# Kernel optimization log

Measured on AMD Instinct MI355X. Metric: run time of the kernel, lower is better.

The kernel has to match this reference:

```python
import jax, jax.numpy as jnp
import numpy as np

F4_E2M1_MAX = 6.0
F8E4M3_MAX = 448.0
E4M3_EPS = 0.015625  # torch.finfo(float8_e4m3fn).tiny = 2**-6
BLOCK = 16
KE2M1 = jnp.array([0.0, 0.5, 1.0, 1.5, 2.0, 3.0, 4.0, 6.0], dtype=jnp.float32)


def round_to_e4m3(x):
    # emulate cast to float8_e4m3fn and back (round-to-nearest-even)
    return x.astype(jnp.float8_e4m3fn).astype(jnp.float32)


def fp4_121_positive(x):
    step1 = jnp.round(2.0 * x) / 2.0   # subnormal-ish region [0,2): step 0.5
    step2 = jnp.round(x)               # [2,4): step 1
    step3 = 2.0 * jnp.round(x / 2.0)   # [4,6]: step 2
    return jnp.where(x < 2.0, step1, jnp.where(x < 4.0, step2, step3))


def cast_to_fp4(x):
    return jnp.sign(x) * fp4_121_positive(jnp.abs(x))


def unpack_fp4_from_uint8(a, m, n):
    # a: int-typed tensor holding byte values in [0,256); two fp4 codes per byte
    high = (a.reshape(-1) >> 4) & 0xF
    low = a.reshape(-1) & 0xF
    combined = jnp.stack((low, high), axis=1).reshape(m, n)  # interleave low,high
    signs = (combined & 8) != 0
    abs_idx = combined & 7
    return KE2M1[abs_idx] * jnp.where(signs, -1.0, 1.0)


def dequant_nvfp4_packed(data_lp, out_scales, per_tensor_scale):
    m, half_n = data_lp.shape
    n = half_n * 2
    data_hp = unpack_fp4_from_uint8(data_lp, m, n)           # [m, n] float32
    scale_fp = out_scales / per_tensor_scale                  # [m, n/16]
    data_hp = data_hp.reshape(m, -1, BLOCK) * scale_fp.reshape(m, -1, 1)
    return data_hp.reshape(m, n)


def qdq_nvfp4(x):
    m, n = x.shape
    tensor_amax = jnp.max(jnp.abs(x))
    pts = jnp.clip(tensor_amax / F8E4M3_MAX, E4M3_EPS, F8E4M3_MAX)  # per-tensor scale
    xb = x.reshape(m, -1, BLOCK)
    block_scale = jnp.max(jnp.abs(xb), axis=-1) / F4_E2M1_MAX       # [m, n/16]
    scaled_bs = round_to_e4m3(jnp.clip(block_scale / pts, E4M3_EPS, F8E4M3_MAX))
    total_scale = pts * scaled_bs                                   # [m, n/16]
    data_scaled = jnp.clip(xb / total_scale[..., None], -F4_E2M1_MAX, F4_E2M1_MAX)
    data_lp = cast_to_fp4(data_scaled)                              # unpacked fp4 values
    # dequant: out_scales / (1/pts) == scaled_bs * pts == total_scale
    return (data_lp * total_scale[..., None]).reshape(m, n)


def setup_inputs() -> dict:
    key = jax.random.key(0)
    k1, k2, k3 = jax.random.split(key, 3)
    M, K, N = 16384, 2048, 2048  # tokens, in_features, out_features
    x = jax.random.normal(k1, (M, K), dtype=jnp.float32)
    weight_packed = jax.random.randint(k2, (N, K // 2), 0, 256, dtype=jnp.int32)
    # fp8-representable positive block scales
    weight_scale = round_to_e4m3(jax.random.uniform(k3, (N, K // 16), dtype=jnp.float32,
                                                    minval=0.05, maxval=1.0))
    weight_global_scale = jnp.ones((1,), dtype=jnp.float32)
    return {"x": x, "weight_packed": weight_packed,
            "weight_scale": weight_scale, "weight_global_scale": weight_global_scale}


def reference(x, weight_packed, weight_scale, weight_global_scale):
    hp_weight = dequant_nvfp4_packed(weight_packed, weight_scale, weight_global_scale)
    x_dq = qdq_nvfp4(x)
    return x_dq @ hp_weight.T
```

## Files before the change

### kernel.cpp

```cpp
#include <hip/hip_runtime.h>

typedef unsigned short u16;
typedef unsigned int u32;
typedef __attribute__((ext_vector_type(8))) short short8;
typedef __attribute__((ext_vector_type(4))) float floatx4;

static constexpr int M = 16384, N = 2048, K = 2048;


__device__ inline u16 f32_to_bf16(float x) {
    u32 u = __float_as_uint(x);
    u += 0x7FFFu + ((u >> 16) & 1u);
    return (u16)(u >> 16);
}

__device__ inline float e4m3_rne(float x) {
    u32 u = __float_as_uint(x);
    u += 0x7FFFFu + ((u >> 20) & 1u);
    u &= 0xFFF00000u;
    return __uint_as_float(u);
}

__device__ inline float fp4_dec(u32 c) {
    u32 e = (c >> 1) & 3u;
    float m = (float)(c & 1u);
    float v = e ? (2.0f + m) * (float)(1u << e) * 0.25f : 0.5f * m;
    return (c & 8u) ? -v : v;
}

__device__ inline float fp4_round_mag(float a) {
    if (a < 2.0f) return rintf(2.0f * a) * 0.5f;
    if (a < 4.0f) return rintf(a);
    return 2.0f * rintf(a * 0.5f);
}

__device__ inline float pts_from_amax(float amax) {
    return fminf(fmaxf(amax / 448.0f, 0.015625f), 448.0f);
}


__global__ void amax_part(const float4* __restrict__ x, float* __restrict__ part, int n4,
                          const int* __restrict__ wp, const float* __restrict__ wsc,
                          const float* __restrict__ wgs, u16* __restrict__ wq) {
    int idx = blockIdx.x * blockDim.x + threadIdx.x;
    int stride = gridDim.x * blockDim.x;
    float m = 0.0f;
    for (int i = idx; i < n4; i += stride) {
        float4 v = x[i];
        m = fmaxf(m, fmaxf(fmaxf(fabsf(v.x), fabsf(v.y)), fmaxf(fabsf(v.z), fabsf(v.w))));
    }

    float ginv = wgs[0];
#pragma unroll
    for (int g = 0; g < 4; g++) {
        int i = idx + g * 524288;
        int n = i >> 10;
        int kb = i & 1023;
        u32 byte = (u32)wp[i] & 0xFFu;
        float scale = wsc[(size_t)n * (K / 16) + (kb >> 3)] / ginv;
        float lo = fp4_dec(byte & 0xFu) * scale;
        float hi = fp4_dec((byte >> 4) & 0xFu) * scale;
        ((u32*)wq)[i] = (u32)f32_to_bf16(lo) | ((u32)f32_to_bf16(hi) << 16);
    }

#pragma unroll
    for (int off = 32; off > 0; off >>= 1)
        m = fmaxf(m, __shfl_down(m, off));
    __shared__ float sm[4];
    if ((threadIdx.x & 63) == 0) sm[threadIdx.x >> 6] = m;
    __syncthreads();
    if (threadIdx.x == 0)
        part[blockIdx.x] = fmaxf(fmaxf(sm[0], sm[1]), fmaxf(sm[2], sm[3]));
}


__global__ void amax_fin(const float* __restrict__ part, u32* __restrict__ out) {
    int t = threadIdx.x;
    float m = fmaxf(part[t], part[t + 1024]);
#pragma unroll
    for (int off = 32; off > 0; off >>= 1)
        m = fmaxf(m, __shfl_down(m, off));
    __shared__ float sm[16];
    if ((t & 63) == 0) sm[t >> 6] = m;
    __syncthreads();
    if (t < 16) {
        m = sm[t];
#pragma unroll
        for (int off = 8; off > 0; off >>= 1)
            m = fmaxf(m, __shfl_down(m, off));
        if (t == 0) *out = __float_as_uint(m);
    }
}


static constexpr int QB = (M * K / 4) / 256;

__global__ void prep(const float4* __restrict__ x, uint2* __restrict__ aq,
                     const u32* __restrict__ amax_bits) {
    int idx = blockIdx.x * blockDim.x + threadIdx.x;
    float4 v = x[idx];

    float bm = fmaxf(fmaxf(fabsf(v.x), fabsf(v.y)), fmaxf(fabsf(v.z), fabsf(v.w)));
    bm = fmaxf(bm, __shfl_xor(bm, 1));
    bm = fmaxf(bm, __shfl_xor(bm, 2));

    float pts = pts_from_amax(__uint_as_float(*amax_bits));
    float bs = bm / 6.0f;
    float sbs = e4m3_rne(fminf(fmaxf(bs / pts, 0.015625f), 448.0f));
    float ts = pts * sbs;

    float vf[4] = {v.x, v.y, v.z, v.w};
    u16 o[4];
#pragma unroll
    for (int i = 0; i < 4; i++) {
        float s = vf[i] / ts;
        s = fminf(fmaxf(s, -6.0f), 6.0f);
        float lp = copysignf(fp4_round_mag(fabsf(s)), s);
        o[i] = f32_to_bf16(lp * sbs);
    }
    aq[idx] = *(const uint2*)o;
}


#define GLDS(g, l)                                                              \
    __builtin_amdgcn_global_load_lds(                                           \
        (const __attribute__((address_space(1))) unsigned int*)(g),             \
        (__attribute__((address_space(3))) unsigned int*)(l), 16, 0, 0)

__global__ __launch_bounds__(512, 2) void gemm_bt(
    const u16* __restrict__ A, const u16* __restrict__ B,
    float* __restrict__ C, const u32* __restrict__ amax_bits, int bm_base)
{
    __shared__ u16 sh[2][2][2][8192];

    const int tid = threadIdx.x;
    const int w = tid >> 6, lane = tid & 63;

    const int id = blockIdx.x;
    const int xcd = id & 7;
    const int local = id >> 3;
    const int bm = bm_base + xcd * 4 + (local >> 3);
    const int bn = local & 7;

    const int wm = w >> 2, wn = w & 3;
    const int r16 = lane & 15, q = lane >> 4;

    floatx4 acc[8][4] = {};

    const int swz = (r16 & 7) << 4;
    const int aoff0 = r16 * 64 + (((q * 16) ^ swz) >> 1);
    const int aoff1 = r16 * 64 + (((64 + q * 16) ^ swz) >> 1);

    const int srow8 = lane >> 3;
    const int scol = ((lane & 7) ^ srow8) * 8;
    const u16* gA[2], * gB[2];
    gA[0] = A + (size_t)(bm * 256 + (w * 2 + 0) * 8 + srow8) * K + scol;
    gA[1] = A + (size_t)(bm * 256 + (w * 2 + 1) * 8 + srow8) * K + scol;
    gB[0] = B + (size_t)(bn * 256 + (w * 2 + 0) * 8 + srow8) * K + scol;
    gB[1] = B + (size_t)(bn * 256 + (w * 2 + 1) * 8 + srow8) * K + scol;

#define STG(buf, mat, half, ktc) do {                                           \
        const u16* _s0 = ((mat) ? gB[0] : gA[0]) + (size_t)(half) * 128 * K + (ktc); \
        const u16* _s1 = ((mat) ? gB[1] : gA[1]) + (size_t)(half) * 128 * K + (ktc); \
        GLDS(_s0, &sh[buf][mat][half][w * 1024]);                               \
        GLDS(_s1, &sh[buf][mat][half][w * 1024 + 512]);                         \
    } while (0)

    short8 aF[4][2], bF[4][2];

#define RD_A(buf, Qa) do {                                                      \
        const u16* _ar = &sh[buf][0][wm][(Qa) * 4096];                          \
        _Pragma("unroll") for (int _i = 0; _i < 4; _i++) {                      \
            aF[_i][0] = *(const short8*)(_ar + _i * 1024 + aoff0);              \
            aF[_i][1] = *(const short8*)(_ar + _i * 1024 + aoff1); }            \
    } while (0)

#define RD_B(buf, Qb) do {                                                      \
        const u16* _br = &sh[buf][1][wn >> 1][(wn & 1) * 4096 + (Qb) * 2048];   \
        _Pragma("unroll") for (int _j = 0; _j < 2; _j++) {                      \
            bF[(Qb) * 2 + _j][0] = *(const short8*)(_br + _j * 1024 + aoff0);   \
            bF[(Qb) * 2 + _j][1] = *(const short8*)(_br + _j * 1024 + aoff1); } \
    } while (0)

#define MMAQ(Qa, Qb)                                                            \
        _Pragma("unroll") for (int _i = 0; _i < 4; _i++)                        \
        _Pragma("unroll") for (int _j = 0; _j < 2; _j++)                        \
        _Pragma("unroll") for (int _k = 0; _k < 2; _k++)                        \
            acc[(Qa) * 4 + _i][(Qb) * 2 + _j] =                                 \
                __builtin_amdgcn_mfma_f32_16x16x32_bf16(                        \
                    aF[_i][_k], bF[(Qb) * 2 + _j][_k],                          \
                    acc[(Qa) * 4 + _i][(Qb) * 2 + _j], 0, 0, 0)

#define BAR do { __builtin_amdgcn_sched_barrier(0);                             \
                 __builtin_amdgcn_s_barrier();                                  \
                 __builtin_amdgcn_sched_barrier(0); } while (0)
#define PRIO1 __builtin_amdgcn_s_setprio(1)
#define PRIO0 do { __builtin_amdgcn_s_setprio(0);                               \
                   __builtin_amdgcn_sched_barrier(0); } while (0)
#define ENDPH do { __builtin_amdgcn_s_barrier();                                \
                   __builtin_amdgcn_sched_barrier(0); } while (0)
#define CHK4 do { asm volatile("s_waitcnt vmcnt(4)" ::: "memory");              \
                  __builtin_amdgcn_sched_barrier(0); } while (0)

    STG(0, 0, 0, 0); STG(0, 0, 1, 0);
    STG(0, 1, 0, 0); STG(0, 1, 1, 0);
    STG(1, 1, 0, 64); STG(1, 1, 1, 64);
    CHK4;
    __builtin_amdgcn_s_barrier();

#pragma unroll 1
    for (int it = 0; it < K / 128; ++it) {
        const int ktY  = (2 * it + 1) * 64;
        const int kx2  = 2 * it + 2, ky2 = 2 * it + 3;
        const int ktX2 = (kx2 <= 31 ? kx2 : 31) * 64;
        const int ktY2 = (ky2 <= 31 ? ky2 : 31) * 64;

        RD_A(0, 0); RD_B(0, 0); STG(1, 0, 0, ktY);
        BAR; PRIO1; MMAQ(0, 0); PRIO0; ENDPH;
        RD_B(0, 1); STG(1, 0, 1, ktY);
        BAR; PRIO1; MMAQ(0, 1); PRIO0; ENDPH;
        RD_A(0, 1); STG(0, 1, 0, ktX2); STG(0, 1, 1, ktX2);
        BAR; PRIO1; MMAQ(1, 1); MMAQ(1, 0); PRIO0; CHK4; ENDPH;
        RD_A(1, 0); RD_B(1, 0); STG(0, 0, 0, ktX2);
        BAR; PRIO1; MMAQ(0, 0); PRIO0; ENDPH;
        RD_B(1, 1); STG(0, 0, 1, ktX2);
        BAR; PRIO1; MMAQ(0, 1); PRIO0; ENDPH;
        RD_A(1, 1); STG(1, 1, 0, ktY2); STG(1, 1, 1, ktY2);
        BAR; PRIO1; MMAQ(1, 1); MMAQ(1, 0); PRIO0; CHK4; ENDPH;
    }

    asm volatile("s_waitcnt vmcnt(0)" ::: "memory");

    float pts = pts_from_amax(__uint_as_float(*amax_bits));

    float* Cb = C + (size_t)(bm * 256 + wm * 128 + q * 4) * N
                  + bn * 256 + wn * 64 + r16;
#pragma unroll
    for (int i = 0; i < 8; i++)
#pragma unroll
        for (int j = 0; j < 4; j++)
#pragma unroll
            for (int t = 0; t < 4; t++)
                Cb[(size_t)(i * 16 + t) * N + j * 16] = pts * acc[i][j][t];
}


extern "C" void kernel_launch(void* const* d_in, const int* in_sizes, int n_in,
                              void* d_out, int out_size, void* d_ws, size_t ws_size,
                              hipStream_t stream) {
    const float* x   = (const float*)d_in[0];
    const int*   wp  = (const int*)d_in[1];
    const float* wsc = (const float*)d_in[2];
    const float* wgs = (const float*)d_in[3];
    float* out = (float*)d_out;

    u32*   amax_ws = (u32*)d_ws;
    float* part    = (float*)((char*)d_ws + 64);
    u16*   aq      = (u16*)((char*)d_ws + 16384);
    u16*   wq      = aq + (size_t)M * K;

    amax_part<<<2048, 256, 0, stream>>>((const float4*)x, part, M * K / 4,
                                        wp, wsc, wgs, wq);
    amax_fin<<<1, 1024, 0, stream>>>(part, amax_ws);
    prep<<<QB, 256, 0, stream>>>((const float4*)x, (uint2*)aq, amax_ws);
    gemm_bt<<<256, 512, 0, stream>>>(aq, wq, out, amax_ws, 0);
    gemm_bt<<<256, 512, 0, stream>>>(aq, wq, out, amax_ws, 32);
}
```

Measured before the change: 385.2 us.

## Fuse amax, quantize, weight dequant and GEMM into one persistent kernel with grid syncs

Replaces the five launches (amax partial, amax final, prep, two GEMM halves) with one persistent 256-block kernel. Software grid barriers built on atomic counters separate the amax/weight-dequant phase, the activation quantization phase and the GEMM phase. Each block then runs two GEMM tiles in sequence and overlaps the first tile's C write with the second tile's prologue. This removes launch gaps and tail effects between kernels, but depends on all 256 blocks being co-resident, adds a memset launch, and the quantization phases now run on only 256 blocks.

```diff
diff --git a/kernel.cpp b/kernel.cpp
--- a/kernel.cpp
+++ b/kernel.cpp
@@ -39,86 +39,16 @@
 }
 
 
-__global__ void amax_part(const float4* __restrict__ x, float* __restrict__ part, int n4,
-                          const int* __restrict__ wp, const float* __restrict__ wsc,
-                          const float* __restrict__ wgs, u16* __restrict__ wq) {
-    int idx = blockIdx.x * blockDim.x + threadIdx.x;
-    int stride = gridDim.x * blockDim.x;
-    float m = 0.0f;
-    for (int i = idx; i < n4; i += stride) {
-        float4 v = x[i];
-        m = fmaxf(m, fmaxf(fmaxf(fabsf(v.x), fabsf(v.y)), fmaxf(fabsf(v.z), fabsf(v.w))));
-    }
-
-    float ginv = wgs[0];
-#pragma unroll
-    for (int g = 0; g < 4; g++) {
-        int i = idx + g * 524288;
-        int n = i >> 10;
-        int kb = i & 1023;
-        u32 byte = (u32)wp[i] & 0xFFu;
-        float scale = wsc[(size_t)n * (K / 16) + (kb >> 3)] / ginv;
-        float lo = fp4_dec(byte & 0xFu) * scale;
-        float hi = fp4_dec((byte >> 4) & 0xFu) * scale;
-        ((u32*)wq)[i] = (u32)f32_to_bf16(lo) | ((u32)f32_to_bf16(hi) << 16);
-    }
-
-#pragma unroll
-    for (int off = 32; off > 0; off >>= 1)
-        m = fmaxf(m, __shfl_down(m, off));
-    __shared__ float sm[4];
-    if ((threadIdx.x & 63) == 0) sm[threadIdx.x >> 6] = m;
+__device__ inline void grid_sync(u32* cnt, u32 target) {
     __syncthreads();
-    if (threadIdx.x == 0)
-        part[blockIdx.x] = fmaxf(fmaxf(sm[0], sm[1]), fmaxf(sm[2], sm[3]));
-}
-
-
-__global__ void amax_fin(const float* __restrict__ part, u32* __restrict__ out) {
-    int t = threadIdx.x;
-    float m = fmaxf(part[t], part[t + 1024]);
-#pragma unroll
-    for (int off = 32; off > 0; off >>= 1)
-        m = fmaxf(m, __shfl_down(m, off));
-    __shared__ float sm[16];
-    if ((t & 63) == 0) sm[t >> 6] = m;
+    __threadfence();
+    if (threadIdx.x == 0) {
+        __hip_atomic_fetch_add(cnt, 1u, __ATOMIC_RELEASE, __HIP_MEMORY_SCOPE_AGENT);
+        while (__hip_atomic_load(cnt, __ATOMIC_ACQUIRE, __HIP_MEMORY_SCOPE_AGENT) < target)
+            __builtin_amdgcn_s_sleep(2);
+    }
     __syncthreads();
-    if (t < 16) {
-        m = sm[t];
-#pragma unroll
-        for (int off = 8; off > 0; off >>= 1)
-            m = fmaxf(m, __shfl_down(m, off));
-        if (t == 0) *out = __float_as_uint(m);
-    }
-}
-
-
-static constexpr int QB = (M * K / 4) / 256;
-
-__global__ void prep(const float4* __restrict__ x, uint2* __restrict__ aq,
-                     const u32* __restrict__ amax_bits) {
-    int idx = blockIdx.x * blockDim.x + threadIdx.x;
-    float4 v = x[idx];
-
-    float bm = fmaxf(fmaxf(fabsf(v.x), fabsf(v.y)), fmaxf(fabsf(v.z), fabsf(v.w)));
-    bm = fmaxf(bm, __shfl_xor(bm, 1));
-    bm = fmaxf(bm, __shfl_xor(bm, 2));
-
-    float pts = pts_from_amax(__uint_as_float(*amax_bits));
-    float bs = bm / 6.0f;
-    float sbs = e4m3_rne(fminf(fmaxf(bs / pts, 0.015625f), 448.0f));
-    float ts = pts * sbs;
-
-    float vf[4] = {v.x, v.y, v.z, v.w};
-    u16 o[4];
-#pragma unroll
-    for (int i = 0; i < 4; i++) {
-        float s = vf[i] / ts;
-        s = fminf(fmaxf(s, -6.0f), 6.0f);
-        float lp = copysignf(fp4_round_mag(fabsf(s)), s);
-        o[i] = f32_to_bf16(lp * sbs);
-    }
-    aq[idx] = *(const uint2*)o;
+    __threadfence();
 }
 
 
@@ -127,19 +57,106 @@
         (const __attribute__((address_space(1))) unsigned int*)(g),             \
         (__attribute__((address_space(3))) unsigned int*)(l), 16, 0, 0)
 
-__global__ __launch_bounds__(512, 2) void gemm_bt(
-    const u16* __restrict__ A, const u16* __restrict__ B,
-    float* __restrict__ C, const u32* __restrict__ amax_bits, int bm_base)
+__global__ __launch_bounds__(512, 2) void mega(
+    const float4* __restrict__ x, const int* __restrict__ wp,
+    const float* __restrict__ wsc, const float* __restrict__ wgs,
+    uint2* __restrict__ aq, u16* __restrict__ wq, float* __restrict__ C,
+    u32* __restrict__ cnt, float* __restrict__ part)
 {
     __shared__ u16 sh[2][2][2][8192];
+    __shared__ float sm8[8];
 
     const int tid = threadIdx.x;
     const int w = tid >> 6, lane = tid & 63;
+    const int gtid = blockIdx.x * 512 + tid;
+
+    {
+        float mx = 0.0f;
+#pragma unroll 4
+        for (int it = 0; it < 64; ++it) {
+            float4 v = x[gtid + it * 131072];
+            mx = fmaxf(mx, fmaxf(fmaxf(fabsf(v.x), fabsf(v.y)),
+                                 fmaxf(fabsf(v.z), fabsf(v.w))));
+        }
+        float ginv = wgs[0];
+#pragma unroll 4
+        for (int g = 0; g < 16; ++g) {
+            int i = gtid + g * 131072;
+            int n = i >> 10;
+            int kb = i & 1023;
+            u32 byte = (u32)wp[i] & 0xFFu;
+            float scale = wsc[(size_t)n * (K / 16) + (kb >> 3)] / ginv;
+            float lo = fp4_dec(byte & 0xFu) * scale;
+            float hi = fp4_dec((byte >> 4) & 0xFu) * scale;
+            ((u32*)wq)[i] = (u32)f32_to_bf16(lo) | ((u32)f32_to_bf16(hi) << 16);
+        }
+#pragma unroll
+        for (int off = 32; off > 0; off >>= 1)
+            mx = fmaxf(mx, __shfl_down(mx, off));
+        if (lane == 0) sm8[w] = mx;
+        __syncthreads();
+        if (tid == 0) {
+            float m = sm8[0];
+#pragma unroll
+            for (int i = 1; i < 8; i++) m = fmaxf(m, sm8[i]);
+            __hip_atomic_store(&part[blockIdx.x], m, __ATOMIC_RELAXED,
+                               __HIP_MEMORY_SCOPE_AGENT);
+        }
+    }
+
+    grid_sync(cnt, 256);
+
+    float pts;
+    {
+        float m = (tid < 256)
+            ? __hip_atomic_load(&part[tid], __ATOMIC_RELAXED, __HIP_MEMORY_SCOPE_AGENT)
+            : 0.0f;
+#pragma unroll
+        for (int off = 32; off > 0; off >>= 1)
+            m = fmaxf(m, __shfl_down(m, off));
+        if (lane == 0) sm8[w] = m;
+        __syncthreads();
+        float amax = sm8[0];
+#pragma unroll
+        for (int i = 1; i < 8; i++) amax = fmaxf(amax, sm8[i]);
+        pts = pts_from_amax(amax);
+
+#pragma unroll 2
+        for (int it = 0; it < 64; ++it) {
+            int idx = gtid + it * 131072;
+            float4 v = x[idx];
+
+            float bm = fmaxf(fmaxf(fabsf(v.x), fabsf(v.y)),
+                             fmaxf(fabsf(v.z), fabsf(v.w)));
+            bm = fmaxf(bm, __shfl_xor(bm, 1));
+            bm = fmaxf(bm, __shfl_xor(bm, 2));
+
+            float bs = bm / 6.0f;
+            float sbs = e4m3_rne(fminf(fmaxf(bs / pts, 0.015625f), 448.0f));
+            float ts = pts * sbs;
+
+            float vf[4] = {v.x, v.y, v.z, v.w};
+            u16 o[4];
+#pragma unroll
+            for (int i = 0; i < 4; i++) {
+                float s = vf[i] / ts;
+                s = fminf(fmaxf(s, -6.0f), 6.0f);
+                float lp = copysignf(fp4_round_mag(fabsf(s)), s);
+                o[i] = f32_to_bf16(lp * sbs);
+            }
+            aq[idx] = *(const uint2*)o;
+        }
+    }
+
+    grid_sync(cnt, 512);
+
+    const u16* A = (const u16*)aq;
+    const u16* B = wq;
 
     const int id = blockIdx.x;
     const int xcd = id & 7;
     const int local = id >> 3;
-    const int bm = bm_base + xcd * 4 + (local >> 3);
+    const int bmbase = xcd * 4 + (local >> 3);
     const int bn = local & 7;
 
     const int wm = w >> 2, wn = w & 3;
@@ -153,9 +170,8 @@
 
     const int srow8 = lane >> 3;
     const int scol = ((lane & 7) ^ srow8) * 8;
-    const u16* gA[2], * gB[2];
-    gA[0] = A + (size_t)(bm * 256 + (w * 2 + 0) * 8 + srow8) * K + scol;
-    gA[1] = A + (size_t)(bm * 256 + (w * 2 + 1) * 8 + srow8) * K + scol;
+    const u16* gA[2];
+    const u16* gB[2];
     gB[0] = B + (size_t)(bn * 256 + (w * 2 + 0) * 8 + srow8) * K + scol;
     gB[1] = B + (size_t)(bn * 256 + (w * 2 + 1) * 8 + srow8) * K + scol;
 
@@ -202,46 +218,61 @@
 #define CHK4 do { asm volatile("s_waitcnt vmcnt(4)" ::: "memory");              \
                   __builtin_amdgcn_sched_barrier(0); } while (0)
 
-    STG(0, 0, 0, 0); STG(0, 0, 1, 0);
-    STG(0, 1, 0, 0); STG(0, 1, 1, 0);
-    STG(1, 1, 0, 64); STG(1, 1, 1, 64);
-    CHK4;
-    __builtin_amdgcn_s_barrier();
+#define CWRITE(bmv) do {                                                        \
+        float* Cb = C + (size_t)((bmv) * 256 + wm * 128 + q * 4) * N            \
+                      + bn * 256 + wn * 64 + r16;                               \
+        _Pragma("unroll") for (int _i = 0; _i < 8; _i++)                        \
+        _Pragma("unroll") for (int _j = 0; _j < 4; _j++)                        \
+        _Pragma("unroll") for (int _t = 0; _t < 4; _t++)                        \
+            Cb[(size_t)(_i * 16 + _t) * N + _j * 16] = pts * acc[_i][_j][_t];   \
+    } while (0)
 
 #pragma unroll 1
-    for (int it = 0; it < K / 128; ++it) {
-        const int ktY  = (2 * it + 1) * 64;
-        const int kx2  = 2 * it + 2, ky2 = 2 * it + 3;
-        const int ktX2 = (kx2 <= 31 ? kx2 : 31) * 64;
-        const int ktY2 = (ky2 <= 31 ? ky2 : 31) * 64;
-
-        RD_A(0, 0); RD_B(0, 0); STG(1, 0, 0, ktY);
-        BAR; PRIO1; MMAQ(0, 0); PRIO0; ENDPH;
-        RD_B(0, 1); STG(1, 0, 1, ktY);
-        BAR; PRIO1; MMAQ(0, 1); PRIO0; ENDPH;
-        RD_A(0, 1); STG(0, 1, 0, ktX2); STG(0, 1, 1, ktX2);
-        BAR; PRIO1; MMAQ(1, 1); MMAQ(1, 0); PRIO0; CHK4; ENDPH;
-        RD_A(1, 0); RD_B(1, 0); STG(0, 0, 0, ktX2);
-        BAR; PRIO1; MMAQ(0, 0); PRIO0; ENDPH;
-        RD_B(1, 1); STG(0, 0, 1, ktX2);
-        BAR; PRIO1; MMAQ(0, 1); PRIO0; ENDPH;
-        RD_A(1, 1); STG(1, 1, 0, ktY2); STG(1, 1, 1, ktY2);
-        BAR; PRIO1; MMAQ(1, 1); MMAQ(1, 0); PRIO0; CHK4; ENDPH;
-    }
-
-    asm volatile("s_waitcnt vmcnt(0)" ::: "memory");
-
-    float pts = pts_from_amax(__uint_as_float(*amax_bits));
-
-    float* Cb = C + (size_t)(bm * 256 + wm * 128 + q * 4) * N
-                  + bn * 256 + wn * 64 + r16;
-#pragma unroll
-    for (int i = 0; i < 8; i++)
-#pragma unroll
-        for (int j = 0; j < 4; j++)
-#pragma unroll
-            for (int t = 0; t < 4; t++)
-                Cb[(size_t)(i * 16 + t) * N + j * 16] = pts * acc[i][j][t];
+    for (int pass = 0; pass < 2; ++pass) {
+        const int bm = bmbase + pass * 32;
+        gA[0] = A + (size_t)(bm * 256 + (w * 2 + 0) * 8 + srow8) * K + scol;
+        gA[1] = A + (size_t)(bm * 256 + (w * 2 + 1) * 8 + srow8) * K + scol;
+
+        STG(0, 0, 0, 0); STG(0, 0, 1, 0);
+        STG(0, 1, 0, 0); STG(0, 1, 1, 0);
+        STG(1, 1, 0, 64); STG(1, 1, 1, 64);
+        CHK4;
+        __builtin_amdgcn_s_barrier();
+
+        if (pass) {
+            CWRITE(bmbase);
+#pragma unroll
+            for (int i = 0; i < 8; i++)
+#pragma unroll
+                for (int j = 0; j < 4; j++)
+                    acc[i][j] = (floatx4){0.f, 0.f, 0.f, 0.f};
+        }
+
+#pragma unroll 1
+        for (int it = 0; it < K / 128; ++it) {
+            const int ktY  = (2 * it + 1) * 64;
+            const int kx2  = 2 * it + 2, ky2 = 2 * it + 3;
+            const int ktX2 = (kx2 <= 31 ? kx2 : 31) * 64;
+            const int ktY2 = (ky2 <= 31 ? ky2 : 31) * 64;
+
+            RD_A(0, 0); RD_B(0, 0); STG(1, 0, 0, ktY);
+            BAR; PRIO1; MMAQ(0, 0); PRIO0; ENDPH;
+            RD_B(0, 1); STG(1, 0, 1, ktY);
+            BAR; PRIO1; MMAQ(0, 1); PRIO0; ENDPH;
+            RD_A(0, 1); STG(0, 1, 0, ktX2); STG(0, 1, 1, ktX2);
+            BAR; PRIO1; MMAQ(1, 1); MMAQ(1, 0); PRIO0; CHK4; ENDPH;
+            RD_A(1, 0); RD_B(1, 0); STG(0, 0, 0, ktX2);
+            BAR; PRIO1; MMAQ(0, 0); PRIO0; ENDPH;
+            RD_B(1, 1); STG(0, 0, 1, ktX2);
+            BAR; PRIO1; MMAQ(0, 1); PRIO0; ENDPH;
+            RD_A(1, 1); STG(1, 1, 0, ktY2); STG(1, 1, 1, ktY2);
+            BAR; PRIO1; MMAQ(1, 1); MMAQ(1, 0); PRIO0; CHK4; ENDPH;
+        }
+
+        asm volatile("s_waitcnt vmcnt(0)" ::: "memory");
+    }
+
+    CWRITE(bmbase + 32);
 }
 
 
@@ -254,15 +285,12 @@
     const float* wgs = (const float*)d_in[3];
     float* out = (float*)d_out;
 
-    u32*   amax_ws = (u32*)d_ws;
-    float* part    = (float*)((char*)d_ws + 64);
-    u16*   aq      = (u16*)((char*)d_ws + 16384);
-    u16*   wq      = aq + (size_t)M * K;
-
-    amax_part<<<2048, 256, 0, stream>>>((const float4*)x, part, M * K / 4,
-                                        wp, wsc, wgs, wq);
-    amax_fin<<<1, 1024, 0, stream>>>(part, amax_ws);
-    prep<<<QB, 256, 0, stream>>>((const float4*)x, (uint2*)aq, amax_ws);
-    gemm_bt<<<256, 512, 0, stream>>>(aq, wq, out, amax_ws, 0);
-    gemm_bt<<<256, 512, 0, stream>>>(aq, wq, out, amax_ws, 32);
-}
+    u32*   cnt  = (u32*)d_ws;
+    float* part = (float*)((char*)d_ws + 64);
+    u16*   aq   = (u16*)((char*)d_ws + 16384);
+    u16*   wq   = aq + (size_t)M * K;
+
+    hipMemsetAsync(d_ws, 0, 64, stream);
+    mega<<<256, 512, 0, stream>>>((const float4*)x, wp, wsc, wgs,
+                                  (uint2*)aq, wq, out, cnt, part);
+}
```

Result: slower. 653.2 us (+69.6%).
